# Kernel tuning notes

Measured on AMD Instinct MI355X. Metric: run time of the kernel, lower is better.

Reference implementation:

```python
import jax, jax.numpy as jnp
import numpy as np
from jax import lax

SIGMOID_THRESH = 0.05  # hard-coded in get_local_max_coords
KERNEL = 3             # default kernel_size


def setup_inputs() -> dict:
    key = jax.random.key(0)
    # [B, num_kps, H, W] heatmap logits from the DeepLab head
    heatmaps = jax.random.normal(key, (16, 17, 384, 384), dtype=jnp.float32)
    return {"heatmaps": heatmaps}


def reference(heatmaps):
    """CenterNet-style local-max peak extraction.

    Faithful to Heatmaps.get_local_max_coords: a pixel is a peak iff it equals
    the 3x3 max-pool of the logits AND sigmoid(logit) > 0.05. Instead of the
    data-dependent torch.nonzero + Python grouping loops (which just reshuffle
    the same information into ragged per-image/per-type lists), we return the
    dense, fixed-shape peak-score map: sigmoid(logit) at peak locations, 0
    elsewhere. The [B, K, H, W] layout already encodes the per-image (axis 0)
    and per-keypoint-type (axis 1) grouping of the original nested loops.
    """
    # 3x3 max-pool, stride 1, SAME padding (pad = kernel // 2)
    max_hm = lax.reduce_window(
        heatmaps,
        -jnp.inf,
        lax.max,
        window_dimensions=(1, 1, KERNEL, KERNEL),
        window_strides=(1, 1, 1, 1),
        padding="SAME",
    )
    prob = jax.nn.sigmoid(heatmaps)
    peak_mask = (max_hm == heatmaps) & (prob > SIGMOID_THRESH)
    return jnp.where(peak_mask, prob, jnp.zeros((), dtype=heatmaps.dtype))
```

## Files before the change

kernel.cpp:

```cpp
#include <hip/hip_runtime.h>
#include <math.h>

#define HH 384
#define WW 384
#define NIMG 272
#define IMG_STRIDE (HH * WW)
#define TW 64
#define TH 64
#define TX 6
#define TY 6
#define NBLOCKS (TX * TY * NIMG)
#define NXCD 8
#define LDS_W 72
#define LDS_H 66
#define ROW_F4 18
#define NL4 (LDS_H * ROW_F4)
#define NLD 5

typedef float f4_t __attribute__((ext_vector_type(4)));

__device__ __forceinline__ float max3f(float a, float b, float c) {
    return fmaxf(fmaxf(a, b), c);
}
__device__ __forceinline__ float fast_sigmoid(float v) {
    return __fdividef(1.0f, 1.0f + __expf(-v));
}

__global__ __launch_bounds__(256, 4) void
heatmap_peaks_tile(const float* __restrict__ in, float* __restrict__ out) {
    __shared__ float S[LDS_H * LDS_W];
    const float NEG = -INFINITY;
    const f4_t NEG4 = {NEG, NEG, NEG, NEG};

    int tid = (int)threadIdx.x;
    int bid = (int)blockIdx.x;
    int swz = (bid % NXCD) * (NBLOCKS / NXCD) + bid / NXCD;

    int txt = swz % TX;
    int tmp = swz / TX;
    int tyt = tmp % TY;
    int img = tmp / TY;
    int x0  = txt * TW;
    int y0  = tyt * TH;

    const float* ib = in + (size_t)img * IMG_STRIDE;

    f4_t va[NLD];
    int  la[NLD];
    bool act[NLD];
#pragma unroll
    for (int k = 0; k < NLD; ++k) {
        int e   = tid + k * 256;
        int row = e / ROW_F4;
        int c4  = e - row * ROW_F4;
        int gy  = y0 - 1 + row;
        int gx  = x0 - 4 + c4 * 4;
        bool vy = (unsigned)gy < (unsigned)HH;
        bool vx = (unsigned)gx <= (unsigned)(WW - 4);
        bool inr = (e < NL4);
        int cy = vy ? gy : 0;
        int cx = vx ? gx : 0;
        f4_t v = *(const f4_t*)(ib + (size_t)cy * WW + cx);
        va[k]  = (vx && vy && inr) ? v : NEG4;
        la[k]  = row * LDS_W + c4 * 4;
        act[k] = inr;
    }
#pragma unroll
    for (int k = 0; k < NLD; ++k)
        if (act[k]) *(f4_t*)&S[la[k]] = va[k];
    __syncthreads();

    int c  = tid & 63;
    int q  = tid >> 6;
    int lc = 4 + c;
    int rbase = q * 16;

    float h[18], val[18];
#pragma unroll
    for (int j = 0; j < 18; ++j) {
        const float* row = &S[(rbase + j) * LDS_W + lc];
        float l = row[-1];
        float m = row[0];
        float r = row[1];
        h[j]   = max3f(l, m, r);
        val[j] = m;
    }

    float* ob = out + (size_t)img * IMG_STRIDE
                    + (size_t)(y0 + rbase) * WW + x0 + c;
#pragma unroll
    for (int j = 0; j < 16; ++j) {
        float m = max3f(h[j], h[j + 1], h[j + 2]);
        float v = val[j + 1];
        float p = fast_sigmoid(v);
        float o = (m == v && p > 0.05f) ? p : 0.0f;
        __builtin_nontemporal_store(o, ob + (size_t)j * WW);
    }
}

extern "C" void kernel_launch(void* const* d_in, const int* in_sizes, int n_in,
                              void* d_out, int out_size, void* d_ws, size_t ws_size,
                              hipStream_t stream) {
    const float* in = (const float*)d_in[0];
    float* out = (float*)d_out;
    heatmap_peaks_tile<<<NBLOCKS, 256, 0, stream>>>(in, out);
}
```

Baseline: 273.0 us.

## Load halo tiles via global_load_lds DMA and compute 4x4 outputs per thread

Replaces the register-staged global-to-LDS tile fill with direct global_load_lds DMA transfers using clamped addresses and a 68-wide LDS row layout. Boundary padding is handled by masking at compute time instead of writing -inf into LDS, with special fixups for the first and last image corners. Each thread now produces a 4x4 output patch with vectorized float4 stores in place of scalar nontemporal stores, and occupancy hint is raised. Edge-handling logic is intricate, which raises correctness risk from misaligned unaligned-by-one row loads and corner fixups.

```diff
diff --git a/kernel.cpp b/kernel.cpp
--- a/kernel.cpp
+++ b/kernel.cpp
@@ -5,17 +5,15 @@
 #define WW 384
 #define NIMG 272
 #define IMG_STRIDE (HH * WW)
+#define NTOT ((long)NIMG * IMG_STRIDE)
 #define TW 64
 #define TH 64
 #define TX 6
 #define TY 6
 #define NBLOCKS (TX * TY * NIMG)
 #define NXCD 8
-#define LDS_W 72
-#define LDS_H 66
-#define ROW_F4 18
-#define NL4 (LDS_H * ROW_F4)
-#define NLD 5
+#define LDS_W 68
+#define NDMA 18
 
 typedef float f4_t __attribute__((ext_vector_type(4)));
 
@@ -26,16 +24,18 @@
     return __fdividef(1.0f, 1.0f + __expf(-v));
 }
 
-__global__ __launch_bounds__(256, 4) void
-heatmap_peaks_tile(const float* __restrict__ in, float* __restrict__ out) {
-    __shared__ float S[LDS_H * LDS_W];
+__global__ __launch_bounds__(256, 6) void
+heatmap_peaks_dma(const float* __restrict__ in, float* __restrict__ out) {
+    __shared__ float S[NDMA * 256];
     const float NEG = -INFINITY;
     const f4_t NEG4 = {NEG, NEG, NEG, NEG};
 
-    int tid = (int)threadIdx.x;
+    int tid  = (int)threadIdx.x;
+    int lane = tid & 63;
+    int wid  = tid >> 6;
+
     int bid = (int)blockIdx.x;
     int swz = (bid % NXCD) * (NBLOCKS / NXCD) + bid / NXCD;
-
     int txt = swz % TX;
     int tmp = swz / TX;
     int tyt = tmp % TY;
@@ -43,58 +43,80 @@
     int x0  = txt * TW;
     int y0  = tyt * TH;
 
-    const float* ib = in + (size_t)img * IMG_STRIDE;
-
-    f4_t va[NLD];
-    int  la[NLD];
-    bool act[NLD];
 #pragma unroll
-    for (int k = 0; k < NLD; ++k) {
-        int e   = tid + k * 256;
-        int row = e / ROW_F4;
-        int c4  = e - row * ROW_F4;
-        int gy  = y0 - 1 + row;
-        int gx  = x0 - 4 + c4 * 4;
-        bool vy = (unsigned)gy < (unsigned)HH;
-        bool vx = (unsigned)gx <= (unsigned)(WW - 4);
-        bool inr = (e < NL4);
-        int cy = vy ? gy : 0;
-        int cx = vx ? gx : 0;
-        f4_t v = *(const f4_t*)(ib + (size_t)cy * WW + cx);
-        va[k]  = (vx && vy && inr) ? v : NEG4;
-        la[k]  = row * LDS_W + c4 * 4;
-        act[k] = inr;
+    for (int i = 0; i < NDMA; ++i) {
+        if ((i & 3) != wid) continue;
+        int chunk    = i * 64 + lane;
+        unsigned row = (unsigned)chunk / 17u;
+        int cin      = chunk - (int)row * 17;
+        int gy       = y0 - 1 + (int)row;
+        gy = gy < 0 ? 0 : (gy > HH - 1 ? HH - 1 : gy);
+        long gidx = (long)img * IMG_STRIDE
+                  + (long)gy * WW + (x0 - 1 + 4 * cin);
+        gidx = gidx < 0 ? 0 : (gidx > NTOT - 4 ? NTOT - 4 : gidx);
+        __builtin_amdgcn_global_load_lds(
+            (const __attribute__((address_space(1))) void*)(in + gidx),
+            (__attribute__((address_space(3))) void*)(S + i * 256),
+            16, 0, 0);
     }
-#pragma unroll
-    for (int k = 0; k < NLD; ++k)
-        if (act[k]) *(f4_t*)&S[la[k]] = va[k];
+    __syncthreads();
+    if (img == 0 && tyt == 0 && txt == 0 && tid == 0) {
+        S[LDS_W + 1] = in[0];
+        S[LDS_W + 2] = in[1];
+        S[LDS_W + 3] = in[2];
+    }
+    if (img == NIMG - 1 && tyt == TY - 1 && txt == TX - 1 && tid == 0)
+        S[64 * LDS_W + 64] = in[NTOT - 1];
     __syncthreads();
 
-    int c  = tid & 63;
-    int q  = tid >> 6;
-    int lc = 4 + c;
-    int rbase = q * 16;
+    int fx = tid & 15;
+    int ry = tid >> 4;
+    const float* Sb = S + ry * 4 * LDS_W + fx * 4;
+    const bool ldead = (fx == 0      && x0 == 0);
+    const bool rdead = (fx == 15     && x0 == WW - TW);
+    const bool tdead = (ry == 0      && y0 == 0);
+    const bool bdead = (ry == 15     && y0 == HH - TH);
 
-    float h[18], val[18];
-#pragma unroll
-    for (int j = 0; j < 18; ++j) {
-        const float* row = &S[(rbase + j) * LDS_W + lc];
-        float l = row[-1];
-        float m = row[0];
-        float r = row[1];
-        h[j]   = max3f(l, m, r);
-        val[j] = m;
-    }
+    auto hrow = [&](int j, f4_t& val) -> f4_t {
+        const float* p = Sb + j * LDS_W;
+        f4_t  b  = *(const f4_t*)p;
+        float c3 = p[4];
+        float rr = p[5];
+        float vl = ldead ? NEG : b.x;
+        float vr = rdead ? NEG : rr;
+        val.x = b.y; val.y = b.z; val.z = b.w; val.w = c3;
+        f4_t h;
+        h.x = max3f(vl,  b.y, b.z);
+        h.y = max3f(b.y, b.z, b.w);
+        h.z = max3f(b.z, b.w, c3);
+        h.w = max3f(b.w, c3,  vr);
+        return h;
+    };
+
+    f4_t vdum;
+    f4_t hA = hrow(0, vdum);
+    if (tdead) hA = NEG4;
+    f4_t vB;
+    f4_t hB = hrow(1, vB);
 
     float* ob = out + (size_t)img * IMG_STRIDE
-                    + (size_t)(y0 + rbase) * WW + x0 + c;
+                    + (size_t)(y0 + ry * 4) * WW + x0 + fx * 4;
 #pragma unroll
-    for (int j = 0; j < 16; ++j) {
-        float m = max3f(h[j], h[j + 1], h[j + 2]);
-        float v = val[j + 1];
-        float p = fast_sigmoid(v);
-        float o = (m == v && p > 0.05f) ? p : 0.0f;
-        __builtin_nontemporal_store(o, ob + (size_t)j * WW);
+    for (int j = 0; j < 4; ++j) {
+        f4_t vC;
+        f4_t hC = hrow(j + 2, vC);
+        if (j == 3 && bdead) hC = NEG4;
+        f4_t o; float m, p;
+        m = max3f(hA.x, hB.x, hC.x); p = fast_sigmoid(vB.x);
+        o.x = (m == vB.x && p > 0.05f) ? p : 0.0f;
+        m = max3f(hA.y, hB.y, hC.y); p = fast_sigmoid(vB.y);
+        o.y = (m == vB.y && p > 0.05f) ? p : 0.0f;
+        m = max3f(hA.z, hB.z, hC.z); p = fast_sigmoid(vB.z);
+        o.z = (m == vB.z && p > 0.05f) ? p : 0.0f;
+        m = max3f(hA.w, hB.w, hC.w); p = fast_sigmoid(vB.w);
+        o.w = (m == vB.w && p > 0.05f) ? p : 0.0f;
+        *(f4_t*)(ob + (size_t)j * WW) = o;
+        hA = hB; hB = hC; vB = vC;
     }
 }
 
@@ -103,5 +125,5 @@
                               hipStream_t stream) {
     const float* in = (const float*)d_in[0];
     float* out = (float*)d_out;
-    heatmap_peaks_tile<<<NBLOCKS, 256, 0, stream>>>(in, out);
+    heatmap_peaks_dma<<<NBLOCKS, 256, 0, stream>>>(in, out);
 }
```

After: 271.0 us. No clear change (-0.7%).
